# Kernel tuning notes

Hardware: AMD Instinct MI355X
Metric: run time of the kernel (lower is better)

Reference implementation:

```python
import jax, jax.numpy as jnp
import numpy as np

POS_R, NEG_MIN_R, NEG_MAX_R, NEG_STEP = 3, 7, 8, 2
CELL_D, BORDER, MAX_NEG_B = 8, 16, 8


def _offsets():
    pos = np.array([(i, j) for i in range(-POS_R, POS_R + 1)
                    for j in range(-POS_R, POS_R + 1)
                    if i * i + j * j <= POS_R ** 2], dtype=np.int32).T  # [2, 29]
    neg = np.array([(i, j) for i in range(-NEG_MAX_R, NEG_MAX_R + 1, NEG_STEP)
                    for j in range(-NEG_MAX_R, NEG_MAX_R + 1, NEG_STEP)
                    if NEG_MIN_R ** 2 <= i * i + j * j <= NEG_MAX_R ** 2], dtype=np.int32).T  # [2, 12]
    return jnp.asarray(pos), jnp.asarray(neg)


def _sample(det, max_b=None):
    # pixel_unshuffle(det[:, :, t:-t, t:-t], cell_d) + argmax over the cell_d^2 channel dim,
    # then decode argmax index back to absolute (x=col, y=row) coordinates.
    B = det.shape[0] if max_b is None else min(max_b, det.shape[0])
    H, W = det.shape[2], det.shape[3]
    d, t = CELL_D, BORDER
    inner = det[:B, 0, t:H - t, t:W - t]                      # [B, Hc, Wc]
    hc, wc = (H - 2 * t) // d, (W - 2 * t) // d
    # pixel_unshuffle channel order is (row_offset i) major, (col_offset j) minor
    cells = inner.reshape(B, hc, d, wc, d).transpose(0, 1, 3, 2, 4).reshape(B, hc, wc, d * d)
    idx = jnp.argmax(cells, axis=-1)                          # [B, hc, wc]
    ii, jj = idx // d, idx % d                                # row / col offsets inside cell
    cy = jnp.arange(hc, dtype=jnp.int32)[None, :, None]
    cx = jnp.arange(wc, dtype=jnp.int32)[None, None, :]
    x = (t + cx * d + jj).reshape(-1)                         # column coordinate (unit_aflow channel 0)
    y = (t + cy * d + ii).reshape(-1)                         # row coordinate   (unit_aflow channel 1)
    n = hc * wc
    b = jnp.repeat(jnp.arange(B, dtype=jnp.int32), n)
    return b, x, y, n


def reference(output1, output2, aflow):
    des1, det1, qlt1 = output1[:, :128], output1[:, 128:129] if False else None, None  # placeholder
    raise NotImplementedError


# NOTE: forward args are the unpacked tensors (see setup_inputs keys)

def _forward(des1, det1, qlt1, des2, det2, qlt2, aflow):
    B, _, H, W = aflow.shape
    pos_off, neg_off = _offsets()
    # original code unpacks sample()'s (b, x, y, n) as (b, y1, x1, n) -- kept faithfully
    b, y1, x1, n = _sample(det1)
    s_des1 = des1[b, :, y1, x1]                               # [N, D]
    xy2 = (aflow[b, :, y1, x1] + 0.5).astype(jnp.int32).T     # [2, N]
    mask = ((0 <= xy2[0]) & (0 <= xy2[1]) & (xy2[0] < W) & (xy2[1] < H)).reshape(B, n)

    def clamp(xy):
        return jnp.stack([jnp.clip(xy[0], 0, W - 1), jnp.clip(xy[1], 0, H - 1)])

    xy2p = clamp(xy2[:, None, :] + pos_off[:, :, None])       # [2, P, N]
    gpos = des2[b, :, xy2p[1], xy2p[0]]                       # [P, N, D]
    pall = jnp.einsum('nd,pnd->np', s_des1, gpos)             # [N, P]
    pos = jnp.argmax(pall, axis=1)                            # [N]
    pscores = jnp.max(pall, axis=1, keepdims=True)            # [N, 1]
    sel_xy2 = clamp(xy2 + pos_off[:, pos])                    # [2, N]
    qlt = (qlt1[b, :, y1, x1] + qlt2[b, :, sel_xy2[1], sel_xy2[0]]) / 2  # [N, 1]

    xy2n = clamp(xy2[:, None, :] + neg_off[:, :, None])       # [2, Q, N]
    nscores = jnp.einsum('nd,qnd->nq', s_des1, des2[b, :, xy2n[1], xy2n[0]])  # [N, Q]

    bd, yd, xd, _ = _sample(det2, MAX_NEG_B)                  # same unpack swap as original
    distr = des2[bd, :, yd, xd]                               # [Nd, D]
    dscores = s_des1 @ distr.T                                # [N, Nd]
    dis2 = (xd[None, :] - xy2[0][:, None]) ** 2 + (yd[None, :] - xy2[1][:, None]) ** 2
    dis2 = dis2 + (bd[None, :] != b[:, None]).astype(jnp.int32) * POS_R ** 2
    dscores = jnp.where(dis2 < POS_R ** 2, 0.0, dscores)

    scores = jnp.concatenate([pscores, nscores, dscores], axis=1)
    labels = jnp.zeros(scores.shape, dtype=bool).at[:, :1].set(True)
    return scores, labels, mask, qlt


def setup_inputs() -> dict:
    key = jax.random.key(0)
    ks = jax.random.split(key, 7)
    B, D, H, W = 8, 128, 256, 256
    des1 = jax.random.normal(ks[0], (B, D, H, W), jnp.float32)
    det1 = jax.random.normal(ks[1], (B, 1, H, W), jnp.float32)
    qlt1 = jax.random.uniform(ks[2], (B, 1, H, W), jnp.float32)
    des2 = jax.random.normal(ks[3], (B, D, H, W), jnp.float32)
    det2 = jax.random.normal(ks[4], (B, 1, H, W), jnp.float32)
    qlt2 = jax.random.uniform(ks[5], (B, 1, H, W), jnp.float32)
    # absolute flow in pixel units, slightly out of range so the validity mask is exercised
    aflow = jax.random.uniform(ks[6], (B, 2, H, W), jnp.float32) * (W + 40.0) - 20.0
    return {"des1": des1, "det1": det1, "qlt1": qlt1,
            "des2": des2, "det2": det2, "qlt2": qlt2, "aflow": aflow}


def reference(des1, det1, qlt1, des2, det2, qlt2, aflow):
    return _forward(des1, det1, qlt1, des2, det2, qlt2, aflow)
```

## Files before the change

### kernel.cpp

```cpp
#include <hip/hip_runtime.h>

typedef unsigned short u16;
typedef unsigned int u32;
typedef __bf16 bf16x8 __attribute__((ext_vector_type(8)));
typedef float f32x4 __attribute__((ext_vector_type(4)));
typedef unsigned int u32x4 __attribute__((ext_vector_type(4)));

#define NS 6272
#define NCOLS 6285
#define SCORES_OFF 0LL
#define LABELS_OFF 39419520LL
#define MASK_OFF   78839040LL
#define QLT_OFF    78845312LL

__constant__ int POSX[29] = {-3,-2,-2,-2,-2,-2,-1,-1,-1,-1,-1, 0,0,0,0,0,0,0, 1,1,1,1,1, 2,2,2,2,2, 3};
__constant__ int POSY[29] = { 0,-2,-1, 0, 1, 2,-2,-1, 0, 1, 2,-3,-2,-1,0,1,2,3,-2,-1,0,1,2,-2,-1,0,1,2, 0};
__constant__ int NEGX[12] = {-8,-6,-6,-4,-4, 0,0, 4,4, 6,6, 8};
__constant__ int NEGY[12] = { 0,-4, 4,-6, 6,-8,8,-6,6,-4,4, 0};

__device__ inline u16 f2bf(float f) {
  u32 u = __float_as_uint(f);
  u = (u + 0x7FFFu + ((u >> 16) & 1u)) >> 16;
  return (u16)u;
}

__global__ __launch_bounds__(256) void sample_kernel(
    const float* __restrict__ det1, const float* __restrict__ det2,
    const float* __restrict__ aflow, const float* __restrict__ qlt1,
    int* __restrict__ sr1, int* __restrict__ sc1,
    int* __restrict__ x2a, int* __restrict__ y2a,
    int* __restrict__ xd, int* __restrict__ yd,
    float* __restrict__ qlt1v, float* __restrict__ out) {
  int isDet2 = (blockIdx.x >= 1568);
  int cell = (blockIdx.x - (isDet2 ? 1568 : 0)) * 4 + (threadIdx.x >> 6);
  int l = threadIdx.x & 63;
  int b = cell / 784, rem = cell % 784;
  int cy = rem / 28, cx = rem % 28;
  int y = 16 + cy * 8 + (l >> 3), x = 16 + cx * 8 + (l & 7);
  const float* det = isDet2 ? det2 : det1;
  float v = det[((size_t)b << 16) + (y << 8) + x];
  int idx = l;
  #pragma unroll
  for (int off = 32; off; off >>= 1) {
    float ov = __shfl_down(v, off);
    int oi = __shfl_down(idx, off);
    if (ov > v || (ov == v && oi < idx)) { v = ov; idx = oi; }
  }
  if (l == 0) {
    int ii = idx >> 3, jj = idx & 7;
    int X = 16 + cx * 8 + jj;
    int Y = 16 + cy * 8 + ii;
    if (!isDet2) {
      sr1[cell] = X; sc1[cell] = Y;
      float ax = aflow[((size_t)(b * 2) << 16) + (X << 8) + Y];
      float ay = aflow[((size_t)(b * 2 + 1) << 16) + (X << 8) + Y];
      int xx = (int)(ax + 0.5f);
      int yy = (int)(ay + 0.5f);
      x2a[cell] = xx; y2a[cell] = yy;
      out[MASK_OFF + cell] = (xx >= 0 && yy >= 0 && xx < 256 && yy < 256) ? 1.0f : 0.0f;
      qlt1v[cell] = qlt1[((size_t)b << 16) + (X << 8) + Y];
    } else {
      yd[cell] = X; xd[cell] = Y;
    }
  }
}

__global__ __launch_bounds__(128) void gather_kernel(
    const float* __restrict__ des1, const float* __restrict__ des2,
    const int* __restrict__ sr1, const int* __restrict__ sc1,
    const int* __restrict__ xd, const int* __restrict__ yd,
    float* __restrict__ A_f32, u16* __restrict__ A_bf16, u16* __restrict__ D_bf16) {
  int i = blockIdx.x, c = threadIdx.x;
  if (i < NS) {
    int n = i, b = n / 784;
    int r = sr1[n], cc = sc1[n];
    float v = des1[(((size_t)b * 128 + c) << 16) + (r << 8) + cc];
    A_f32[(size_t)n * 128 + c] = v;
    A_bf16[(size_t)n * 128 + c] = f2bf(v);
  } else {
    int m = i - NS, b = m / 784;
    int r = yd[m], cc = xd[m];
    float v = des2[(((size_t)b * 128 + c) << 16) + (r << 8) + cc];
    D_bf16[(size_t)m * 128 + c] = f2bf(v);
  }
}

__global__ __launch_bounds__(256) void small_scores_kernel(
    const float* __restrict__ des2, const float* __restrict__ qlt2,
    const float* __restrict__ A_f32, const int* __restrict__ x2a,
    const int* __restrict__ y2a, const float* __restrict__ qlt1v,
    float* __restrict__ out) {
  int n = blockIdx.x * 4 + (threadIdx.x >> 6);
  int l = threadIdx.x & 63;
  int b = n / 784;
  int x2 = x2a[n], y2 = y2a[n];
  int ox = 0, oy = 0;
  if (l < 29) { ox = POSX[l]; oy = POSY[l]; }
  else if (l < 41) { ox = NEGX[l - 29]; oy = NEGY[l - 29]; }
  int xc = min(max(x2 + ox, 0), 255);
  int yc = min(max(y2 + oy, 0), 255);
  const float* d2 = des2 + ((size_t)b << 23) + ((size_t)yc << 8) + xc;
  const float* ar = A_f32 + (size_t)n * 128;
  float acc = 0.0f;
  #pragma unroll 16
  for (int c = 0; c < 128; ++c) acc += ar[c] * d2[(size_t)c << 16];
  if (l >= 29 && l < 41) out[SCORES_OFF + (size_t)n * NCOLS + 1 + (l - 29)] = acc;
  float v = (l < 29) ? acc : -1e30f;
  int idx = l;
  #pragma unroll
  for (int off = 32; off; off >>= 1) {
    float ov = __shfl_down(v, off);
    int oi = __shfl_down(idx, off);
    if (ov > v || (ov == v && oi < idx)) { v = ov; idx = oi; }
  }
  if (l == 0) {
    out[SCORES_OFF + (size_t)n * NCOLS] = v;
    int sx = min(max(x2 + POSX[idx], 0), 255);
    int sy = min(max(y2 + POSY[idx], 0), 255);
    float q = (qlt1v[n] + qlt2[((size_t)b << 16) + (sy << 8) + sx]) * 0.5f;
    out[QLT_OFF + n] = q;
  }
}

__global__ __launch_bounds__(256) void labels_kernel(float* __restrict__ out) {
  int n = blockIdx.x * 256 + threadIdx.x;
  if (n < NS) out[LABELS_OFF + (size_t)n * NCOLS] = 1.0f;
}

__global__ __launch_bounds__(256, 2) void gemm_kernel(
    const u16* __restrict__ A, const u16* __restrict__ Bm,
    const int* __restrict__ x2a, const int* __restrict__ y2a,
    const int* __restrict__ xd, const int* __restrict__ yd,
    float* __restrict__ out) {
  __shared__ u16 As[128 * 136];
  __shared__ u16 Bs[128 * 136];
  int tid = threadIdx.x;
  int R = blockIdx.y, C = blockIdx.x;
  const u32x4* gA = (const u32x4*)(A + (size_t)R * 16384);
  const u32x4* gB = (const u32x4*)(Bm + (size_t)C * 16384);
  #pragma unroll
  for (int p = 0; p < 8; ++p) {
    int i = tid + p * 256;
    int r = i >> 4, kc = (i & 15) * 8;
    *(u32x4*)&As[r * 136 + kc] = gA[i];
    *(u32x4*)&Bs[r * 136 + kc] = gB[i];
  }
  __syncthreads();
  int l = tid & 63, w = tid >> 6;
  int lr = l & 15, lq = l >> 4;
  int wr = (w & 1) * 64, wc = (w >> 1) * 64;
  f32x4 acc[4][4] = {};
  #pragma unroll
  for (int kk = 0; kk < 4; ++kk) {
    bf16x8 af[4], bfr[4];
    #pragma unroll
    for (int t = 0; t < 4; ++t) {
      af[t]  = *(const bf16x8*)&As[(wr + t * 16 + lr) * 136 + kk * 32 + lq * 8];
      bfr[t] = *(const bf16x8*)&Bs[(wc + t * 16 + lr) * 136 + kk * 32 + lq * 8];
    }
    #pragma unroll
    for (int tr = 0; tr < 4; ++tr)
      #pragma unroll
      for (int tc = 0; tc < 4; ++tc)
        acc[tr][tc] = __builtin_amdgcn_mfma_f32_16x16x32_bf16(af[tr], bfr[tc], acc[tr][tc], 0, 0, 0);
  }
  #pragma unroll
  for (int tr = 0; tr < 4; ++tr) {
    int rows[4], rx[4], ry[4], rb[4];
    #pragma unroll
    for (int r = 0; r < 4; ++r) {
      int row = R * 128 + wr + tr * 16 + lq * 4 + r;
      rows[r] = row; rx[r] = x2a[row]; ry[r] = y2a[row]; rb[r] = row / 784;
    }
    #pragma unroll
    for (int tc = 0; tc < 4; ++tc) {
      int col = C * 128 + wc + tc * 16 + lr;
      int cxv = xd[col], cyv = yd[col], cb = col / 784;
      #pragma unroll
      for (int r = 0; r < 4; ++r) {
        int dx = cxv - rx[r], dy = cyv - ry[r];
        int dis2 = dx * dx + dy * dy + (cb != rb[r] ? 9 : 0);
        float v = acc[tr][tc][r];
        if (dis2 < 9) v = 0.0f;
        out[SCORES_OFF + (size_t)rows[r] * NCOLS + 13 + col] = v;
      }
    }
  }
}

extern "C" void kernel_launch(void* const* d_in, const int* in_sizes, int n_in,
                              void* d_out, int out_size, void* d_ws, size_t ws_size,
                              hipStream_t stream) {
  const float* des1 = (const float*)d_in[0];
  const float* det1 = (const float*)d_in[1];
  const float* qlt1 = (const float*)d_in[2];
  const float* des2 = (const float*)d_in[3];
  const float* det2 = (const float*)d_in[4];
  const float* qlt2 = (const float*)d_in[5];
  const float* aflow = (const float*)d_in[6];
  float* out = (float*)d_out;

  char* ws = (char*)d_ws;
  int* sr1 = (int*)ws;
  int* sc1 = sr1 + NS;
  int* x2a = sc1 + NS;
  int* y2a = x2a + NS;
  int* xd  = y2a + NS;
  int* yd  = xd + NS;
  float* qlt1v = (float*)(yd + NS);
  float* A_f32 = qlt1v + NS;
  u16* A_bf16 = (u16*)(A_f32 + (size_t)NS * 128);
  u16* D_bf16 = A_bf16 + (size_t)NS * 128;

  hipMemsetAsync((void*)(out + LABELS_OFF), 0, (size_t)NS * NCOLS * sizeof(float), stream);

  sample_kernel<<<3136, 256, 0, stream>>>(det1, det2, aflow, qlt1,
                                          sr1, sc1, x2a, y2a, xd, yd, qlt1v, out);
  gather_kernel<<<2 * NS, 128, 0, stream>>>(des1, des2, sr1, sc1, xd, yd,
                                            A_f32, A_bf16, D_bf16);
  small_scores_kernel<<<NS / 4, 256, 0, stream>>>(des2, qlt2, A_f32, x2a, y2a, qlt1v, out);
  labels_kernel<<<(NS + 255) / 256, 256, 0, stream>>>(out);
  dim3 g(49, 49);
  gemm_kernel<<<g, 256, 0, stream>>>(A_bf16, D_bf16, x2a, y2a, xd, yd, out);
}
```

Baseline: 778.9 us.

## Fuse five launches into two kernels with in-kernel zeroing and nontemporal stores

After: 811.9 us. 1.04x slower.

```diff
diff --git a/kernel.cpp b/kernel.cpp
--- a/kernel.cpp
+++ b/kernel.cpp
@@ -13,6 +13,9 @@
 #define MASK_OFF   78839040LL
 #define QLT_OFF    78845312LL
 
+#define ZBLK 2048
+#define LBL_F4 9854880
+
 __constant__ int POSX[29] = {-3,-2,-2,-2,-2,-2,-1,-1,-1,-1,-1, 0,0,0,0,0,0,0, 1,1,1,1,1, 2,2,2,2,2, 3};
 __constant__ int POSY[29] = { 0,-2,-1, 0, 1, 2,-2,-1, 0, 1, 2,-3,-2,-1,0,1,2,3,-2,-1,0,1,2,-2,-1,0,1,2, 0};
 __constant__ int NEGX[12] = {-8,-6,-6,-4,-4, 0,0, 4,4, 6,6, 8};
@@ -24,13 +27,23 @@
   return (u16)u;
 }
 
-__global__ __launch_bounds__(256) void sample_kernel(
+__global__ __launch_bounds__(256) void sample_gather_zero_kernel(
     const float* __restrict__ det1, const float* __restrict__ det2,
     const float* __restrict__ aflow, const float* __restrict__ qlt1,
-    int* __restrict__ sr1, int* __restrict__ sc1,
+    const float* __restrict__ des1, const float* __restrict__ des2,
     int* __restrict__ x2a, int* __restrict__ y2a,
     int* __restrict__ xd, int* __restrict__ yd,
-    float* __restrict__ qlt1v, float* __restrict__ out) {
+    float* __restrict__ qlt1v,
+    float* __restrict__ A_f32, u16* __restrict__ A_bf16, u16* __restrict__ D_bf16,
+    float* __restrict__ out) {
+  if (blockIdx.x >= 3136) {
+    size_t t = (size_t)(blockIdx.x - 3136) * 256 + threadIdx.x;
+    f32x4* p = (f32x4*)(out + LABELS_OFF);
+    f32x4 z = {0.0f, 0.0f, 0.0f, 0.0f};
+    for (size_t i = t; i < (size_t)LBL_F4; i += (size_t)ZBLK * 256)
+      __builtin_nontemporal_store(z, p + i);
+    return;
+  }
   int isDet2 = (blockIdx.x >= 1568);
   int cell = (blockIdx.x - (isDet2 ? 1568 : 0)) * 4 + (threadIdx.x >> 6);
   int l = threadIdx.x & 63;
@@ -41,17 +54,16 @@
   float v = det[((size_t)b << 16) + (y << 8) + x];
   int idx = l;
   #pragma unroll
-  for (int off = 32; off; off >>= 1) {
-    float ov = __shfl_down(v, off);
-    int oi = __shfl_down(idx, off);
+  for (int off = 1; off < 64; off <<= 1) {
+    float ov = __shfl_xor(v, off);
+    int oi = __shfl_xor(idx, off);
     if (ov > v || (ov == v && oi < idx)) { v = ov; idx = oi; }
   }
-  if (l == 0) {
-    int ii = idx >> 3, jj = idx & 7;
-    int X = 16 + cx * 8 + jj;
-    int Y = 16 + cy * 8 + ii;
-    if (!isDet2) {
-      sr1[cell] = X; sc1[cell] = Y;
+  int ii = idx >> 3, jj = idx & 7;
+  int X = 16 + cx * 8 + jj;
+  int Y = 16 + cy * 8 + ii;
+  if (!isDet2) {
+    if (l == 0) {
       float ax = aflow[((size_t)(b * 2) << 16) + (X << 8) + Y];
       float ay = aflow[((size_t)(b * 2 + 1) << 16) + (X << 8) + Y];
       int xx = (int)(ax + 0.5f);
@@ -59,83 +71,70 @@
       x2a[cell] = xx; y2a[cell] = yy;
       out[MASK_OFF + cell] = (xx >= 0 && yy >= 0 && xx < 256 && yy < 256) ? 1.0f : 0.0f;
       qlt1v[cell] = qlt1[((size_t)b << 16) + (X << 8) + Y];
-    } else {
+    }
+    const float* p = des1 + (((size_t)b * 128) << 16) + (X << 8) + Y;
+    float v0 = p[(size_t)l << 16];
+    float v1 = p[(size_t)(l + 64) << 16];
+    A_f32[(size_t)cell * 128 + l] = v0;
+    A_f32[(size_t)cell * 128 + l + 64] = v1;
+    A_bf16[(size_t)cell * 128 + l] = f2bf(v0);
+    A_bf16[(size_t)cell * 128 + l + 64] = f2bf(v1);
+  } else {
+    if (l == 0) {
       yd[cell] = X; xd[cell] = Y;
     }
-  }
-}
-
-__global__ __launch_bounds__(128) void gather_kernel(
-    const float* __restrict__ des1, const float* __restrict__ des2,
-    const int* __restrict__ sr1, const int* __restrict__ sc1,
-    const int* __restrict__ xd, const int* __restrict__ yd,
-    float* __restrict__ A_f32, u16* __restrict__ A_bf16, u16* __restrict__ D_bf16) {
-  int i = blockIdx.x, c = threadIdx.x;
-  if (i < NS) {
-    int n = i, b = n / 784;
-    int r = sr1[n], cc = sc1[n];
-    float v = des1[(((size_t)b * 128 + c) << 16) + (r << 8) + cc];
-    A_f32[(size_t)n * 128 + c] = v;
-    A_bf16[(size_t)n * 128 + c] = f2bf(v);
-  } else {
-    int m = i - NS, b = m / 784;
-    int r = yd[m], cc = xd[m];
-    float v = des2[(((size_t)b * 128 + c) << 16) + (r << 8) + cc];
-    D_bf16[(size_t)m * 128 + c] = f2bf(v);
-  }
-}
-
-__global__ __launch_bounds__(256) void small_scores_kernel(
+    const float* p = des2 + (((size_t)b * 128) << 16) + (X << 8) + Y;
+    D_bf16[(size_t)cell * 128 + l] = f2bf(p[(size_t)l << 16]);
+    D_bf16[(size_t)cell * 128 + l + 64] = f2bf(p[(size_t)(l + 64) << 16]);
+  }
+}
+
+__global__ __launch_bounds__(256, 2) void scores_kernel(
+    const u16* __restrict__ A, const u16* __restrict__ Bm,
     const float* __restrict__ des2, const float* __restrict__ qlt2,
-    const float* __restrict__ A_f32, const int* __restrict__ x2a,
-    const int* __restrict__ y2a, const float* __restrict__ qlt1v,
-    float* __restrict__ out) {
-  int n = blockIdx.x * 4 + (threadIdx.x >> 6);
-  int l = threadIdx.x & 63;
-  int b = n / 784;
-  int x2 = x2a[n], y2 = y2a[n];
-  int ox = 0, oy = 0;
-  if (l < 29) { ox = POSX[l]; oy = POSY[l]; }
-  else if (l < 41) { ox = NEGX[l - 29]; oy = NEGY[l - 29]; }
-  int xc = min(max(x2 + ox, 0), 255);
-  int yc = min(max(y2 + oy, 0), 255);
-  const float* d2 = des2 + ((size_t)b << 23) + ((size_t)yc << 8) + xc;
-  const float* ar = A_f32 + (size_t)n * 128;
-  float acc = 0.0f;
-  #pragma unroll 16
-  for (int c = 0; c < 128; ++c) acc += ar[c] * d2[(size_t)c << 16];
-  if (l >= 29 && l < 41) out[SCORES_OFF + (size_t)n * NCOLS + 1 + (l - 29)] = acc;
-  float v = (l < 29) ? acc : -1e30f;
-  int idx = l;
-  #pragma unroll
-  for (int off = 32; off; off >>= 1) {
-    float ov = __shfl_down(v, off);
-    int oi = __shfl_down(idx, off);
-    if (ov > v || (ov == v && oi < idx)) { v = ov; idx = oi; }
-  }
-  if (l == 0) {
-    out[SCORES_OFF + (size_t)n * NCOLS] = v;
-    int sx = min(max(x2 + POSX[idx], 0), 255);
-    int sy = min(max(y2 + POSY[idx], 0), 255);
-    float q = (qlt1v[n] + qlt2[((size_t)b << 16) + (sy << 8) + sx]) * 0.5f;
-    out[QLT_OFF + n] = q;
-  }
-}
-
-__global__ __launch_bounds__(256) void labels_kernel(float* __restrict__ out) {
-  int n = blockIdx.x * 256 + threadIdx.x;
-  if (n < NS) out[LABELS_OFF + (size_t)n * NCOLS] = 1.0f;
-}
-
-__global__ __launch_bounds__(256, 2) void gemm_kernel(
-    const u16* __restrict__ A, const u16* __restrict__ Bm,
+    const float* __restrict__ A_f32, const float* __restrict__ qlt1v,
     const int* __restrict__ x2a, const int* __restrict__ y2a,
     const int* __restrict__ xd, const int* __restrict__ yd,
     float* __restrict__ out) {
   __shared__ u16 As[128 * 136];
   __shared__ u16 Bs[128 * 136];
   int tid = threadIdx.x;
-  int R = blockIdx.y, C = blockIdx.x;
+  if (blockIdx.x < 1568) {
+    int n = blockIdx.x * 4 + (tid >> 6);
+    int l = tid & 63;
+    int b = n / 784;
+    int x2 = x2a[n], y2 = y2a[n];
+    int ox = 0, oy = 0;
+    if (l < 29) { ox = POSX[l]; oy = POSY[l]; }
+    else if (l < 41) { ox = NEGX[l - 29]; oy = NEGY[l - 29]; }
+    int xc = min(max(x2 + ox, 0), 255);
+    int yc = min(max(y2 + oy, 0), 255);
+    const float* d2 = des2 + ((size_t)b << 23) + ((size_t)yc << 8) + xc;
+    const float* ar = A_f32 + (size_t)n * 128;
+    float acc = 0.0f;
+    #pragma unroll 16
+    for (int c = 0; c < 128; ++c) acc += ar[c] * d2[(size_t)c << 16];
+    if (l >= 29 && l < 41) out[SCORES_OFF + (size_t)n * NCOLS + 1 + (l - 29)] = acc;
+    float v = (l < 29) ? acc : -1e30f;
+    int idx = l;
+    #pragma unroll
+    for (int off = 32; off; off >>= 1) {
+      float ov = __shfl_down(v, off);
+      int oi = __shfl_down(idx, off);
+      if (ov > v || (ov == v && oi < idx)) { v = ov; idx = oi; }
+    }
+    if (l == 0) {
+      out[SCORES_OFF + (size_t)n * NCOLS] = v;
+      out[LABELS_OFF + (size_t)n * NCOLS] = 1.0f;
+      int sx = min(max(x2 + POSX[idx], 0), 255);
+      int sy = min(max(y2 + POSY[idx], 0), 255);
+      float q = (qlt1v[n] + qlt2[((size_t)b << 16) + (sy << 8) + sx]) * 0.5f;
+      out[QLT_OFF + n] = q;
+    }
+    return;
+  }
+  int bi = blockIdx.x - 1568;
+  int R = bi / 49, C = bi % 49;
   const u32x4* gA = (const u32x4*)(A + (size_t)R * 16384);
   const u32x4* gB = (const u32x4*)(Bm + (size_t)C * 16384);
   #pragma unroll
@@ -182,7 +181,7 @@
         int dis2 = dx * dx + dy * dy + (cb != rb[r] ? 9 : 0);
         float v = acc[tr][tc][r];
         if (dis2 < 9) v = 0.0f;
-        out[SCORES_OFF + (size_t)rows[r] * NCOLS + 13 + col] = v;
+        __builtin_nontemporal_store(v, &out[SCORES_OFF + (size_t)rows[r] * NCOLS + 13 + col]);
       }
     }
   }
@@ -201,25 +200,19 @@
   float* out = (float*)d_out;
 
   char* ws = (char*)d_ws;
-  int* sr1 = (int*)ws;
-  int* sc1 = sr1 + NS;
-  int* x2a = sc1 + NS;
+  int* x2a = (int*)ws;
   int* y2a = x2a + NS;
   int* xd  = y2a + NS;
   int* yd  = xd + NS;
   float* qlt1v = (float*)(yd + NS);
-  float* A_f32 = qlt1v + NS;
+  float* A_f32 = qlt1v + NS + NS;
   u16* A_bf16 = (u16*)(A_f32 + (size_t)NS * 128);
   u16* D_bf16 = A_bf16 + (size_t)NS * 128;
 
-  hipMemsetAsync((void*)(out + LABELS_OFF), 0, (size_t)NS * NCOLS * sizeof(float), stream);
-
-  sample_kernel<<<3136, 256, 0, stream>>>(det1, det2, aflow, qlt1,
-                                          sr1, sc1, x2a, y2a, xd, yd, qlt1v, out);
-  gather_kernel<<<2 * NS, 128, 0, stream>>>(des1, des2, sr1, sc1, xd, yd,
-                                            A_f32, A_bf16, D_bf16);
-  small_scores_kernel<<<NS / 4, 256, 0, stream>>>(des2, qlt2, A_f32, x2a, y2a, qlt1v, out);
-  labels_kernel<<<(NS + 255) / 256, 256, 0, stream>>>(out);
-  dim3 g(49, 49);
-  gemm_kernel<<<g, 256, 0, stream>>>(A_bf16, D_bf16, x2a, y2a, xd, yd, out);
-}
+  sample_gather_zero_kernel<<<3136 + ZBLK, 256, 0, stream>>>(
+      det1, det2, aflow, qlt1, des1, des2,
+      x2a, y2a, xd, yd, qlt1v, A_f32, A_bf16, D_bf16, out);
+
+  scores_kernel<<<1568 + 49 * 49, 256, 0, stream>>>(
+      A_bf16, D_bf16, des2, qlt2, A_f32, qlt1v, x2a, y2a, xd, yd, out);
+}
```
